# Kernel tuning notes

Hardware: AMD Instinct MI355X
Metric: run time of the kernel (lower is better)

## Reference

```python
import jax, jax.numpy as jnp
import numpy as np

N_NODES = 50000
N_EDGES = 800000
IN_F = 128
HEADS = 4
OUT_F = 32
NEG_SLOPE = 0.2


def setup_inputs() -> dict:
    key = jax.random.key(0)
    k1, k2, k3, k4 = jax.random.split(key, 4)
    x = jax.random.normal(k1, (1, N_NODES, IN_F), dtype=jnp.float32)
    edge_index = jax.random.randint(k2, (2, N_EDGES), 0, N_NODES, dtype=jnp.int64)
    # nn.Linear(in, heads*out, bias=False): weight shape [heads*out, in]
    W = jax.random.normal(k3, (HEADS * OUT_F, IN_F), dtype=jnp.float32) * 0.05
    att = jax.random.normal(k4, (1, HEADS, 2 * OUT_F), dtype=jnp.float32) * 0.05
    bias = jnp.zeros((HEADS * OUT_F,), dtype=jnp.float32)
    return {"x": x, "edge_index": edge_index, "W": W, "att": att, "bias": bias}


def reference(x, edge_index, W, att, bias):
    B, n, _ = x.shape
    # h = W(x) -> [B, N, H, F]
    h = (x @ W.T).reshape(B, n, HEADS, OUT_F)
    # add self loops
    loops = jnp.arange(n, dtype=edge_index.dtype)
    src = jnp.concatenate([edge_index[0], loops])
    dst = jnp.concatenate([edge_index[1], loops])
    # attention scores: leaky_relu(cat(h_src, h_dst)) . att  -> [B, Etot, H]
    h_cat = jnp.concatenate([h[:, src], h[:, dst]], axis=-1)  # [B, Etot, H, 2F]
    att_in = jax.nn.leaky_relu(h_cat, NEG_SLOPE)
    scores = jnp.sum(att_in * att, axis=-1)  # att [1,H,2F] broadcasts -> [B, Etot, H]
    # NOTE: faithful to the original: softmax over the FULL edge axis (dim=1),
    # not a per-destination segment softmax.
    w = jax.nn.softmax(scores, axis=1)  # [B, Etot, H]
    # aggregate: scatter-add weighted source features to destination nodes
    weighted = h[:, src] * w[..., None]  # [B, Etot, H, F]
    out = jax.vmap(lambda wf: jax.ops.segment_sum(wf, dst, num_segments=n))(weighted)
    # [B, N, H, F] -> [B, N, H*F] + bias
    return out.reshape(B, n, HEADS * OUT_F) + bias
```

## Files before the change

kernel.cpp:

```cpp
#include <hip/hip_runtime.h>
#include <math.h>

#define N_NODES 50000
#define N_EDGES 800000
#define E_TOT   850000
#define IN_F    128
#define HEADS   4
#define OUT_F   32
#define HF      128
#define NEG_SLOPE 0.2f
#define ELLW    40
#define OVF_CAP 4096
#define DEN_SLOTS 16
#define NXCD    8
#define DPX     6250

#define WS_G      0
#define WS_ES     3200000
#define WS_ED     3400000
#define WS_DEN    3600000
#define WS_CNT    3610000
#define WS_ELL    3660000
#define WS_OVFC   4660000
#define WS_OVFS   4660064
#define WS_OVFD   4664160
#define NBLK_EDGE 3321

static __device__ __forceinline__ float4 ld4(const float* p) {
    return *reinterpret_cast<const float4*>(p);
}
static __device__ __forceinline__ unsigned short f2bf(float f) {
    unsigned u = __float_as_uint(f);
    return (unsigned short)((u + 0x7FFFu + ((u >> 16) & 1u)) >> 16);
}
static __device__ __forceinline__ float4 bf2f4(ushort4 v) {
    return make_float4(__uint_as_float((unsigned)v.x << 16),
                       __uint_as_float((unsigned)v.y << 16),
                       __uint_as_float((unsigned)v.z << 16),
                       __uint_as_float((unsigned)v.w << 16));
}

__global__ __launch_bounds__(256) void k_gemm_attprep(
    const float* __restrict__ x, const float* __restrict__ W,
    const float* __restrict__ att, unsigned short* __restrict__ g,
    float* __restrict__ es, float* __restrict__ ed,
    int* __restrict__ cnt, int* __restrict__ ovf_cnt,
    float* __restrict__ denom)
{
    __shared__ float wt[32 * 128];
    const int t  = threadIdx.x;
    const int n0 = blockIdx.x * 32;

    if (t < 32) {
        int z = n0 + t;
        if (z < N_NODES) cnt[z] = 0;
    }
    if (blockIdx.x == 0) {
        if (t == 0) *ovf_cnt = 0;
        if (t < DEN_SLOTS * 4) denom[t] = 0.f;
    }

    const int cg = t & 31;
    const int nr = t >> 5;
    float4 acc[4];
    #pragma unroll
    for (int ni = 0; ni < 4; ++ni) acc[ni] = make_float4(0.f, 0.f, 0.f, 0.f);

    const float4* wt4 = reinterpret_cast<const float4*>(wt);
    const float4* x4  = reinterpret_cast<const float4*>(x);

    int row[4];
    #pragma unroll
    for (int ni = 0; ni < 4; ++ni) {
        int n = n0 + nr + ni * 8;
        row[ni] = n < N_NODES ? n : N_NODES - 1;
    }

    for (int kt = 0; kt < 4; ++kt) {
        __syncthreads();
        {
            const int c = t >> 1, half = t & 1;
            #pragma unroll
            for (int i = 0; i < 4; ++i) {
                float4 wv = ld4(W + c * 128 + kt * 32 + half * 16 + i * 4);
                int kk = half * 16 + i * 4;
                wt[(kk + 0) * 128 + c] = wv.x;
                wt[(kk + 1) * 128 + c] = wv.y;
                wt[(kk + 2) * 128 + c] = wv.z;
                wt[(kk + 3) * 128 + c] = wv.w;
            }
        }
        __syncthreads();

        #pragma unroll
        for (int kk4 = 0; kk4 < 8; ++kk4) {
            float xv[4][4];
            #pragma unroll
            for (int ni = 0; ni < 4; ++ni)
                *reinterpret_cast<float4*>(xv[ni]) =
                    x4[row[ni] * 32 + kt * 8 + kk4];
            #pragma unroll
            for (int j = 0; j < 4; ++j) {
                float4 wv = wt4[(kk4 * 4 + j) * 32 + cg];
                #pragma unroll
                for (int ni = 0; ni < 4; ++ni) {
                    acc[ni].x += xv[ni][j] * wv.x;
                    acc[ni].y += xv[ni][j] * wv.y;
                    acc[ni].z += xv[ni][j] * wv.z;
                    acc[ni].w += xv[ni][j] * wv.w;
                }
            }
        }
    }

    const int head = cg >> 3;
    const int f0   = (cg & 7) * 4;
    float4 as = ld4(att + head * 64 + f0);
    float4 ad = ld4(att + head * 64 + 32 + f0);

    #pragma unroll
    for (int ni = 0; ni < 4; ++ni) {
        int n = n0 + nr + ni * 8;
        if (n < N_NODES) {
            float lx = acc[ni].x > 0.f ? acc[ni].x : NEG_SLOPE * acc[ni].x;
            float ly = acc[ni].y > 0.f ? acc[ni].y : NEG_SLOPE * acc[ni].y;
            float lz = acc[ni].z > 0.f ? acc[ni].z : NEG_SLOPE * acc[ni].z;
            float lw = acc[ni].w > 0.f ? acc[ni].w : NEG_SLOPE * acc[ni].w;
            float ps = lx * as.x + ly * as.y + lz * as.z + lw * as.w;
            float pd = lx * ad.x + ly * ad.y + lz * ad.z + lw * ad.w;
            ps += __shfl_xor(ps, 1); ps += __shfl_xor(ps, 2); ps += __shfl_xor(ps, 4);
            pd += __shfl_xor(pd, 1); pd += __shfl_xor(pd, 2); pd += __shfl_xor(pd, 4);
            float esv = expf(ps);
            ushort4 sv;
            sv.x = f2bf(acc[ni].x * esv);
            sv.y = f2bf(acc[ni].y * esv);
            sv.z = f2bf(acc[ni].z * esv);
            sv.w = f2bf(acc[ni].w * esv);
            *reinterpret_cast<ushort4*>(&g[n * 128 + cg * 4]) = sv;
            if ((t & 7) == 0) {
                es[n * 4 + head] = esv;
                ed[n * 4 + head] = expf(pd);
            }
        }
    }
}

__global__ __launch_bounds__(256) void k_edge_fill_denom(
    const int* __restrict__ eidx, const float* __restrict__ es,
    const float* __restrict__ ed, int* __restrict__ cnt,
    unsigned short* __restrict__ ell, int* __restrict__ ovf_cnt,
    int* __restrict__ ovf_s, int* __restrict__ ovf_d,
    float* __restrict__ denom)
{
    __shared__ float4 red[256];
    const int t     = threadIdx.x;
    const int chunk = blockIdx.x >> 3;
    const int xcd   = blockIdx.x & 7;
    const int e     = chunk * 256 + t;

    if (e < N_EDGES) {
        int d = eidx[N_EDGES + e];
        if (d >= xcd * DPX && d < (xcd + 1) * DPX) {
            int s = eidx[e];
            int pos = atomicAdd(&cnt[d], 1);
            if (pos < ELLW) {
                ell[d * ELLW + pos] = (unsigned short)s;
            } else {
                int o = atomicAdd(ovf_cnt, 1);
                if (o < OVF_CAP) { ovf_s[o] = s; ovf_d[o] = d; }
            }
        }
    }

    if (xcd == 0) {
        float4 w = make_float4(0.f, 0.f, 0.f, 0.f);
        if (e < E_TOT) {
            int s, d;
            if (e < N_EDGES) { s = eidx[e]; d = eidx[N_EDGES + e]; }
            else             { s = d = e - N_EDGES; }
            float4 vs = ld4(es + s * 4);
            float4 vd = ld4(ed + d * 4);
            w.x = vs.x * vd.x;
            w.y = vs.y * vd.y;
            w.z = vs.z * vd.z;
            w.w = vs.w * vd.w;
        }
        red[t] = w;
        __syncthreads();
        for (int sdt = 128; sdt > 0; sdt >>= 1) {
            if (t < sdt) {
                float4 o = red[t + sdt];
                red[t].x += o.x; red[t].y += o.y; red[t].z += o.z; red[t].w += o.w;
            }
            __syncthreads();
        }
        if (t < 4)
            atomicAdd(&denom[(chunk & (DEN_SLOTS - 1)) * 4 + t],
                      reinterpret_cast<const float*>(&red[0])[t]);
    }
}

__global__ __launch_bounds__(256) void k_gather(
    const int* __restrict__ cnt, const unsigned short* __restrict__ ell,
    const float* __restrict__ ed, const unsigned short* __restrict__ g,
    const float* __restrict__ denom, const float* __restrict__ bias,
    const int* __restrict__ ovf_cnt, const int* __restrict__ ovf_s,
    const int* __restrict__ ovf_d, float* __restrict__ out)
{
    const int t = threadIdx.x;
    const int n = blockIdx.x * 8 + (t >> 5);
    if (n >= N_NODES) return;
    const int lane = t & 31;
    const int head = lane >> 3;

    const ushort4* g4 = reinterpret_cast<const ushort4*>(g);

    float4 acc = bf2f4(g4[n * 32 + lane]);

    const int raw = cnt[n];
    const int deg = min(raw, ELLW);
    const unsigned short* __restrict__ row = ell + n * ELLW;
    int j = 0;
    for (; j + 3 < deg; j += 4) {
        int s0 = row[j],     s1 = row[j + 1];
        int s2 = row[j + 2], s3 = row[j + 3];
        float4 g0 = bf2f4(g4[s0 * 32 + lane]);
        float4 g1 = bf2f4(g4[s1 * 32 + lane]);
        float4 g2 = bf2f4(g4[s2 * 32 + lane]);
        float4 g3 = bf2f4(g4[s3 * 32 + lane]);
        acc.x += g0.x + g1.x + g2.x + g3.x;
        acc.y += g0.y + g1.y + g2.y + g3.y;
        acc.z += g0.z + g1.z + g2.z + g3.z;
        acc.w += g0.w + g1.w + g2.w + g3.w;
    }
    for (; j < deg; ++j) {
        int s0 = row[j];
        float4 g0 = bf2f4(g4[s0 * 32 + lane]);
        acc.x += g0.x; acc.y += g0.y; acc.z += g0.z; acc.w += g0.w;
    }

    if (raw > ELLW) {
        int m = min(*ovf_cnt, OVF_CAP);
        for (int i = 0; i < m; ++i) {
            if (ovf_d[i] == n) {
                float4 g0 = bf2f4(g4[ovf_s[i] * 32 + lane]);
                acc.x += g0.x; acc.y += g0.y; acc.z += g0.z; acc.w += g0.w;
            }
        }
    }

    float dsum = 0.f;
    #pragma unroll
    for (int i2 = 0; i2 < DEN_SLOTS; ++i2) dsum += denom[i2 * 4 + head];

    const float sc = ed[n * 4 + head] / dsum;
    float4 b = ld4(bias + lane * 4);
    float4 o = make_float4(acc.x * sc + b.x, acc.y * sc + b.y,
                           acc.z * sc + b.z, acc.w * sc + b.w);
    *reinterpret_cast<float4*>(out + n * 128 + lane * 4) = o;
}

extern "C" void kernel_launch(void* const* d_in, const int* in_sizes, int n_in,
                              void* d_out, int out_size, void* d_ws, size_t ws_size,
                              hipStream_t stream) {
    const float* x    = (const float*)d_in[0];
    const int*   eidx = (const int*)d_in[1];
    const float* W    = (const float*)d_in[2];
    const float* att  = (const float*)d_in[3];
    const float* bias = (const float*)d_in[4];
    float* out = (float*)d_out;
    float* ws  = (float*)d_ws;

    unsigned short* g   = (unsigned short*)(ws + WS_G);
    float* es     = ws + WS_ES;
    float* ed     = ws + WS_ED;
    float* denom  = ws + WS_DEN;
    int*   cnt    = (int*)(ws + WS_CNT);
    unsigned short* ell = (unsigned short*)(ws + WS_ELL);
    int*   ovfc   = (int*)(ws + WS_OVFC);
    int*   ovfs   = (int*)(ws + WS_OVFS);
    int*   ovfd   = (int*)(ws + WS_OVFD);

    k_gemm_attprep   <<<(N_NODES + 31) / 32, 256, 0, stream>>>(x, W, att, g, es, ed, cnt, ovfc, denom);
    k_edge_fill_denom<<<NBLK_EDGE * NXCD,    256, 0, stream>>>(eidx, es, ed, cnt, ell, ovfc, ovfs, ovfd, denom);
    k_gather         <<<(N_NODES + 7) / 8,   256, 0, stream>>>(cnt, ell, ed, g, denom, bias, ovfc, ovfs, ovfd, out);
}
```

Measured before the change: 228.6 us.

## Use bf16 MFMA for projection GEMM and drop XCD-partitioned edge fill

```diff
diff --git a/kernel.cpp b/kernel.cpp
--- a/kernel.cpp
+++ b/kernel.cpp
@@ -12,8 +12,6 @@
 #define ELLW    40
 #define OVF_CAP 4096
 #define DEN_SLOTS 16
-#define NXCD    8
-#define DPX     6250
 
 #define WS_G      0
 #define WS_ES     3200000
@@ -26,6 +24,9 @@
 #define WS_OVFD   4664160
 #define NBLK_EDGE 3321
 
+typedef __attribute__((ext_vector_type(8))) short bf16x8;
+typedef __attribute__((ext_vector_type(4))) float f32x4;
+
 static __device__ __forceinline__ float4 ld4(const float* p) {
     return *reinterpret_cast<const float4*>(p);
 }
@@ -47,11 +48,11 @@
     int* __restrict__ cnt, int* __restrict__ ovf_cnt,
     float* __restrict__ denom)
 {
-    __shared__ float wt[32 * 128];
+    __shared__ unsigned short wbf[128 * 128];
     const int t  = threadIdx.x;
-    const int n0 = blockIdx.x * 32;
-
-    if (t < 32) {
+    const int n0 = blockIdx.x * 64;
+
+    if (t < 64) {
         int z = n0 + t;
         if (z < N_NODES) cnt[z] = 0;
     }
@@ -60,86 +61,93 @@
         if (t < DEN_SLOTS * 4) denom[t] = 0.f;
     }
 
-    const int cg = t & 31;
-    const int nr = t >> 5;
-    float4 acc[4];
-    #pragma unroll
-    for (int ni = 0; ni < 4; ++ni) acc[ni] = make_float4(0.f, 0.f, 0.f, 0.f);
-
-    const float4* wt4 = reinterpret_cast<const float4*>(wt);
-    const float4* x4  = reinterpret_cast<const float4*>(x);
-
-    int row[4];
-    #pragma unroll
-    for (int ni = 0; ni < 4; ++ni) {
-        int n = n0 + nr + ni * 8;
-        row[ni] = n < N_NODES ? n : N_NODES - 1;
-    }
-
+    {
+        const int c  = t >> 1;
+        const int kh = (t & 1) * 8;
+        #pragma unroll
+        for (int i = 0; i < 8; ++i) {
+            int k8 = kh + i;
+            float4 a = ld4(W + c * 128 + k8 * 8);
+            float4 b = ld4(W + c * 128 + k8 * 8 + 4);
+            ushort4 lo, hi;
+            lo.x = f2bf(a.x); lo.y = f2bf(a.y); lo.z = f2bf(a.z); lo.w = f2bf(a.w);
+            hi.x = f2bf(b.x); hi.y = f2bf(b.y); hi.z = f2bf(b.z); hi.w = f2bf(b.w);
+            int byteoff = c * 256 + ((k8 * 16) ^ ((c & 7) << 4));
+            *reinterpret_cast<ushort4*>((char*)wbf + byteoff)     = lo;
+            *reinterpret_cast<ushort4*>((char*)wbf + byteoff + 8) = hi;
+        }
+    }
+    __syncthreads();
+
+    const int w = t >> 6;
+    const int l = t & 63;
+    const int li = l & 15;
+    const int lk = l >> 4;
+
+    int arow = n0 + w * 16 + li;
+    if (arow >= N_NODES) arow = N_NODES - 1;
+
+    f32x4 acc[8];
+    #pragma unroll
+    for (int ct = 0; ct < 8; ++ct) acc[ct] = (f32x4){0.f, 0.f, 0.f, 0.f};
+
+    #pragma unroll
     for (int kt = 0; kt < 4; ++kt) {
-        __syncthreads();
-        {
-            const int c = t >> 1, half = t & 1;
+        const float* xp = x + arow * 128 + kt * 32 + lk * 8;
+        float4 a = ld4(xp), b = ld4(xp + 4);
+        bf16x8 af;
+        af[0] = (short)f2bf(a.x); af[1] = (short)f2bf(a.y);
+        af[2] = (short)f2bf(a.z); af[3] = (short)f2bf(a.w);
+        af[4] = (short)f2bf(b.x); af[5] = (short)f2bf(b.y);
+        af[6] = (short)f2bf(b.z); af[7] = (short)f2bf(b.w);
+        #pragma unroll
+        for (int ct = 0; ct < 8; ++ct) {
+            int col = ct * 16 + li;
+            int k8  = kt * 4 + lk;
+            int byteoff = col * 256 + ((k8 * 16) ^ ((col & 7) << 4));
+            bf16x8 bf = *reinterpret_cast<const bf16x8*>((const char*)wbf + byteoff);
+            acc[ct] = __builtin_amdgcn_mfma_f32_16x16x32_bf16(af, bf, acc[ct], 0, 0, 0);
+        }
+    }
+
+    float as_[8], ad_[8];
+    #pragma unroll
+    for (int ct = 0; ct < 8; ++ct) {
+        int col = ct * 16 + li;
+        int hd = col >> 5, f = col & 31;
+        as_[ct] = att[hd * 64 + f];
+        ad_[ct] = att[hd * 64 + 32 + f];
+    }
+
+    #pragma unroll
+    for (int j = 0; j < 4; ++j) {
+        int n = n0 + w * 16 + lk * 4 + j;
+        float ps[4] = {0.f, 0.f, 0.f, 0.f};
+        float pd[4] = {0.f, 0.f, 0.f, 0.f};
+        #pragma unroll
+        for (int ct = 0; ct < 8; ++ct) {
+            float v  = acc[ct][j];
+            float lv = v > 0.f ? v : NEG_SLOPE * v;
+            ps[ct >> 1] += lv * as_[ct];
+            pd[ct >> 1] += lv * ad_[ct];
+        }
+        #pragma unroll
+        for (int hd = 0; hd < 4; ++hd) {
+            ps[hd] += __shfl_xor(ps[hd], 1); ps[hd] += __shfl_xor(ps[hd], 2);
+            ps[hd] += __shfl_xor(ps[hd], 4); ps[hd] += __shfl_xor(ps[hd], 8);
+            pd[hd] += __shfl_xor(pd[hd], 1); pd[hd] += __shfl_xor(pd[hd], 2);
+            pd[hd] += __shfl_xor(pd[hd], 4); pd[hd] += __shfl_xor(pd[hd], 8);
+        }
+        if (n < N_NODES) {
+            float esv[4];
             #pragma unroll
-            for (int i = 0; i < 4; ++i) {
-                float4 wv = ld4(W + c * 128 + kt * 32 + half * 16 + i * 4);
-                int kk = half * 16 + i * 4;
-                wt[(kk + 0) * 128 + c] = wv.x;
-                wt[(kk + 1) * 128 + c] = wv.y;
-                wt[(kk + 2) * 128 + c] = wv.z;
-                wt[(kk + 3) * 128 + c] = wv.w;
-            }
-        }
-        __syncthreads();
-
-        #pragma unroll
-        for (int kk4 = 0; kk4 < 8; ++kk4) {
-            float xv[4][4];
+            for (int hd = 0; hd < 4; ++hd) esv[hd] = expf(ps[hd]);
             #pragma unroll
-            for (int ni = 0; ni < 4; ++ni)
-                *reinterpret_cast<float4*>(xv[ni]) =
-                    x4[row[ni] * 32 + kt * 8 + kk4];
-            #pragma unroll
-            for (int j = 0; j < 4; ++j) {
-                float4 wv = wt4[(kk4 * 4 + j) * 32 + cg];
-                #pragma unroll
-                for (int ni = 0; ni < 4; ++ni) {
-                    acc[ni].x += xv[ni][j] * wv.x;
-                    acc[ni].y += xv[ni][j] * wv.y;
-                    acc[ni].z += xv[ni][j] * wv.z;
-                    acc[ni].w += xv[ni][j] * wv.w;
-                }
-            }
-        }
-    }
-
-    const int head = cg >> 3;
-    const int f0   = (cg & 7) * 4;
-    float4 as = ld4(att + head * 64 + f0);
-    float4 ad = ld4(att + head * 64 + 32 + f0);
-
-    #pragma unroll
-    for (int ni = 0; ni < 4; ++ni) {
-        int n = n0 + nr + ni * 8;
-        if (n < N_NODES) {
-            float lx = acc[ni].x > 0.f ? acc[ni].x : NEG_SLOPE * acc[ni].x;
-            float ly = acc[ni].y > 0.f ? acc[ni].y : NEG_SLOPE * acc[ni].y;
-            float lz = acc[ni].z > 0.f ? acc[ni].z : NEG_SLOPE * acc[ni].z;
-            float lw = acc[ni].w > 0.f ? acc[ni].w : NEG_SLOPE * acc[ni].w;
-            float ps = lx * as.x + ly * as.y + lz * as.z + lw * as.w;
-            float pd = lx * ad.x + ly * ad.y + lz * ad.z + lw * ad.w;
-            ps += __shfl_xor(ps, 1); ps += __shfl_xor(ps, 2); ps += __shfl_xor(ps, 4);
-            pd += __shfl_xor(pd, 1); pd += __shfl_xor(pd, 2); pd += __shfl_xor(pd, 4);
-            float esv = expf(ps);
-            ushort4 sv;
-            sv.x = f2bf(acc[ni].x * esv);
-            sv.y = f2bf(acc[ni].y * esv);
-            sv.z = f2bf(acc[ni].z * esv);
-            sv.w = f2bf(acc[ni].w * esv);
-            *reinterpret_cast<ushort4*>(&g[n * 128 + cg * 4]) = sv;
-            if ((t & 7) == 0) {
-                es[n * 4 + head] = esv;
-                ed[n * 4 + head] = expf(pd);
+            for (int ct = 0; ct < 8; ++ct)
+                g[n * 128 + ct * 16 + li] = f2bf(acc[ct][j] * esv[ct >> 1]);
+            if (li < 4) {
+                es[n * 4 + li] = esv[li];
+                ed[n * 4 + li] = expf(pd[li]);
             }
         }
     }
@@ -153,15 +161,13 @@
     float* __restrict__ denom)
 {
     __shared__ float4 red[256];
-    const int t     = threadIdx.x;
-    const int chunk = blockIdx.x >> 3;
-    const int xcd   = blockIdx.x & 7;
-    const int e     = chunk * 256 + t;
-
-    if (e < N_EDGES) {
-        int d = eidx[N_EDGES + e];
-        if (d >= xcd * DPX && d < (xcd + 1) * DPX) {
-            int s = eidx[e];
+    const int t = threadIdx.x;
+    const int e = blockIdx.x * 256 + t;
+    float4 w = make_float4(0.f, 0.f, 0.f, 0.f);
+    if (e < E_TOT) {
+        int s, d;
+        if (e < N_EDGES) {
+            s = eidx[e]; d = eidx[N_EDGES + e];
             int pos = atomicAdd(&cnt[d], 1);
             if (pos < ELLW) {
                 ell[d * ELLW + pos] = (unsigned short)s;
@@ -169,35 +175,28 @@
                 int o = atomicAdd(ovf_cnt, 1);
                 if (o < OVF_CAP) { ovf_s[o] = s; ovf_d[o] = d; }
             }
-        }
-    }
-
-    if (xcd == 0) {
-        float4 w = make_float4(0.f, 0.f, 0.f, 0.f);
-        if (e < E_TOT) {
-            int s, d;
-            if (e < N_EDGES) { s = eidx[e]; d = eidx[N_EDGES + e]; }
-            else             { s = d = e - N_EDGES; }
-            float4 vs = ld4(es + s * 4);
-            float4 vd = ld4(ed + d * 4);
-            w.x = vs.x * vd.x;
-            w.y = vs.y * vd.y;
-            w.z = vs.z * vd.z;
-            w.w = vs.w * vd.w;
-        }
-        red[t] = w;
+        } else {
+            s = d = e - N_EDGES;
+        }
+        float4 vs = ld4(es + s * 4);
+        float4 vd = ld4(ed + d * 4);
+        w.x = vs.x * vd.x;
+        w.y = vs.y * vd.y;
+        w.z = vs.z * vd.z;
+        w.w = vs.w * vd.w;
+    }
+    red[t] = w;
+    __syncthreads();
+    for (int sdt = 128; sdt > 0; sdt >>= 1) {
+        if (t < sdt) {
+            float4 o = red[t + sdt];
+            red[t].x += o.x; red[t].y += o.y; red[t].z += o.z; red[t].w += o.w;
+        }
         __syncthreads();
-        for (int sdt = 128; sdt > 0; sdt >>= 1) {
-            if (t < sdt) {
-                float4 o = red[t + sdt];
-                red[t].x += o.x; red[t].y += o.y; red[t].z += o.z; red[t].w += o.w;
-            }
-            __syncthreads();
-        }
-        if (t < 4)
-            atomicAdd(&denom[(chunk & (DEN_SLOTS - 1)) * 4 + t],
-                      reinterpret_cast<const float*>(&red[0])[t]);
-    }
+    }
+    if (t < 4)
+        atomicAdd(&denom[(blockIdx.x & (DEN_SLOTS - 1)) * 4 + t],
+                  reinterpret_cast<const float*>(&red[0])[t]);
 }
 
 __global__ __launch_bounds__(256) void k_gather(
@@ -281,7 +280,7 @@
     int*   ovfs   = (int*)(ws + WS_OVFS);
     int*   ovfd   = (int*)(ws + WS_OVFD);
 
-    k_gemm_attprep   <<<(N_NODES + 31) / 32, 256, 0, stream>>>(x, W, att, g, es, ed, cnt, ovfc, denom);
-    k_edge_fill_denom<<<NBLK_EDGE * NXCD,    256, 0, stream>>>(eidx, es, ed, cnt, ell, ovfc, ovfs, ovfd, denom);
+    k_gemm_attprep   <<<(N_NODES + 63) / 64, 256, 0, stream>>>(x, W, att, g, es, ed, cnt, ovfc, denom);
+    k_edge_fill_denom<<<NBLK_EDGE,           256, 0, stream>>>(eidx, es, ed, cnt, ell, ovfc, ovfs, ovfd, denom);
     k_gather         <<<(N_NODES + 7) / 8,   256, 0, stream>>>(cnt, ell, ed, g, denom, bias, ovfc, ovfs, ovfd, out);
 }
```

Result: faster. 187.7 us (-17.9%).
